# Optimization experiments

Measured on AMD Instinct MI355X. Metric: run time of the kernel, lower is better.

## Reference

```python
import jax, jax.numpy as jnp
import numpy as np
import math

B, N, F_IN, F_OUT = 8, 2048, 128, 128


def _uniform(key, shape, stdv):
    return jax.random.uniform(key, shape, dtype=jnp.float32, minval=-stdv, maxval=stdv)


def setup_inputs() -> dict:
    key = jax.random.key(0)
    k_x, k_a, k_w, k_att, k_bw, k_ba = jax.random.split(key, 6)
    X = jax.random.normal(k_x, (B, N, F_IN), dtype=jnp.float32)
    # dense 0/1 adjacency, as consumed by torch.bmm(A, ...)
    A = jax.random.randint(k_a, (B, N, N), 0, 2).astype(jnp.float32)
    stdv_W = 1.0 / math.sqrt(F_OUT)        # W.size(1) == n_fea_out
    stdv_a = 1.0 / math.sqrt(2 * F_OUT)    # a.size(1) == 2*n_fea_out
    W = _uniform(k_w, (F_IN, F_OUT), stdv_W)
    a = _uniform(k_att, (1, 2 * F_OUT), stdv_a)
    bias_W = _uniform(k_bw, (F_OUT,), stdv_W)
    bias_a = _uniform(k_ba, (N,), stdv_a)
    return {"X": X, "A": A, "W": W, "a": a, "bias_a": bias_a, "bias_W": bias_W}


def reference(X, A, W, a, bias_a, bias_W):
    # XW: [B, N, F_out]
    XW = jnp.einsum('bnf,fo->bno', X, W)
    f = W.shape[1]
    # Original materializes Z[b,i,j] = concat(XW[b,j], XW[b,i]) then dots with a.
    # This is separable: Z1[b,i,j] = a[:f]@XW[b,j] + a[f:]@XW[b,i] + bias_a[j]
    a_j = a[0, :f]   # multiplies XW[b, j]
    a_i = a[0, f:]   # multiplies XW[b, i]
    s_j = jnp.einsum('bnf,f->bn', XW, a_j)  # [B, N]
    s_i = jnp.einsum('bnf,f->bn', XW, a_i)  # [B, N]
    Z1 = s_i[:, :, None] + s_j[:, None, :] + bias_a[None, None, :]  # [B, N, N]
    den = jnp.exp(Z1)
    num = jnp.einsum('bik,bkj->bij', A, den)  # torch.bmm(A, denominator)
    # where numerator == 0 the torch code leaves att uninitialized; use 0 deterministically
    nz = num != 0
    att = jnp.where(nz, den / jnp.where(nz, num, 1.0), 0.0)
    buf = jnp.einsum('bij,bjf->bif', att, XW)
    H = jnp.einsum('bij,bjf->bif', A, buf) + bias_W
    return H
```

## Files before the change

kernel.cpp:

```cpp
#include <hip/hip_runtime.h>

#define BB 8
#define NN 2048
#define FF 128


__global__ __launch_bounds__(128) void k0_wai(const float* __restrict__ W,
                                              const float* __restrict__ a,
                                              float* __restrict__ w_ai) {
    int c = threadIdx.x;
    float s = 0.f;
#pragma unroll 8
    for (int f = 0; f < FF; ++f) s += W[c * FF + f] * a[FF + f];
    w_ai[c] = s;
}

__global__ __launch_bounds__(256) void k1_p_xsum(const float* __restrict__ X,
                                                 const float* __restrict__ w_ai,
                                                 float* __restrict__ p,
                                                 float* __restrict__ xsum) {
    int blk = blockIdx.x;
    int b = blk / (NN / 64);
    int row0 = (blk % (NN / 64)) * 64;
    int lane = threadIdx.x & 63;
    int wave = threadIdx.x >> 6;

    const float2* X2 = (const float2*)(X + ((size_t)b * NN + row0) * FF);
    float2 wv = ((const float2*)w_ai)[lane];
    float csx = 0.f, csy = 0.f;

    for (int it = 0; it < 16; ++it) {
        int rloc = wave * 16 + it;
        float2 xv = X2[(size_t)rloc * 64 + lane];
        csx += xv.x;
        csy += xv.y;
        float s = xv.x * wv.x + xv.y * wv.y;
#pragma unroll
        for (int off = 32; off; off >>= 1) s += __shfl_xor(s, off, 64);
        if (lane == 0) p[(size_t)b * NN + row0 + rloc] = expf(s);
    }

    __shared__ float cs_lds[4][FF];
    cs_lds[wave][lane * 2]     = csx;
    cs_lds[wave][lane * 2 + 1] = csy;
    __syncthreads();
    if (threadIdx.x < FF) {
        float v = cs_lds[0][threadIdx.x] + cs_lds[1][threadIdx.x] +
                  cs_lds[2][threadIdx.x] + cs_lds[3][threadIdx.x];
        atomicAdd(&xsum[b * FF + threadIdx.x], v);
    }
}

__global__ __launch_bounds__(128) void k2_S(const float* __restrict__ W,
                                            const float* __restrict__ xsum,
                                            float* __restrict__ S) {
    int b = blockIdx.x;
    int f = threadIdx.x;
    float s = 0.f;
#pragma unroll 8
    for (int c = 0; c < FF; ++c) s += xsum[b * FF + c] * W[c * FF + f];
    S[b * FF + f] = s;
}

__global__ __launch_bounds__(256) void k3_r(const float* __restrict__ A,
                                            const float* __restrict__ p,
                                            float* __restrict__ r) {
    __shared__ float p_lds[NN];
    int row0 = blockIdx.x * 4;
    int b = row0 >> 11;

    const float4* p4 = (const float4*)(p + (size_t)b * NN);
    ((float4*)p_lds)[threadIdx.x]       = p4[threadIdx.x];
    ((float4*)p_lds)[threadIdx.x + 256] = p4[threadIdx.x + 256];
    __syncthreads();

    int lane = threadIdx.x & 63;
    int wave = threadIdx.x >> 6;
    int row = row0 + wave;
    const float4* A4 = (const float4*)(A + (size_t)row * NN);

    float acc = 0.f;
#pragma unroll
    for (int it = 0; it < 8; ++it) {
        float4 av = A4[it * 64 + lane];
        float4 pv = *(const float4*)&p_lds[it * 256 + lane * 4];
        acc += av.x * pv.x + av.y * pv.y + av.z * pv.z + av.w * pv.w;
    }
#pragma unroll
    for (int off = 32; off; off >>= 1) acc += __shfl_xor(acc, off, 64);

    if (lane == 0) {
        int i = row & (NN - 1);
        r[row] = (acc != 0.f) ? (p_lds[i] / acc) : 0.f;
    }
}

__global__ __launch_bounds__(256) void k4_H(const float* __restrict__ A,
                                            const float* __restrict__ rr,
                                            const float* __restrict__ S,
                                            const float* __restrict__ bias_W,
                                            float* __restrict__ Hout) {
    __shared__ float r_lds[NN];
    __shared__ float s_lds[FF];
    __shared__ float bw_lds[FF];
    int row0 = blockIdx.x * 4;
    int b = row0 >> 11;

    const float4* r4 = (const float4*)(rr + (size_t)b * NN);
    ((float4*)r_lds)[threadIdx.x]       = r4[threadIdx.x];
    ((float4*)r_lds)[threadIdx.x + 256] = r4[threadIdx.x + 256];
    if (threadIdx.x < FF) {
        s_lds[threadIdx.x]  = S[b * FF + threadIdx.x];
        bw_lds[threadIdx.x] = bias_W[threadIdx.x];
    }
    __syncthreads();

    int lane = threadIdx.x & 63;
    int wave = threadIdx.x >> 6;
    int row = row0 + wave;
    const float4* A4 = (const float4*)(A + (size_t)row * NN);

    float acc = 0.f;
#pragma unroll
    for (int it = 0; it < 8; ++it) {
        float4 av = A4[it * 64 + lane];
        float4 rv = *(const float4*)&r_lds[it * 256 + lane * 4];
        acc += av.x * rv.x + av.y * rv.y + av.z * rv.z + av.w * rv.w;
    }
#pragma unroll
    for (int off = 32; off; off >>= 1) acc += __shfl_xor(acc, off, 64);

    float2 sv = ((const float2*)s_lds)[lane];
    float2 bv = ((const float2*)bw_lds)[lane];
    float2 hv;
    hv.x = acc * sv.x + bv.x;
    hv.y = acc * sv.y + bv.y;
    ((float2*)Hout)[(size_t)row * 64 + lane] = hv;
}

extern "C" void kernel_launch(void* const* d_in, const int* in_sizes, int n_in,
                              void* d_out, int out_size, void* d_ws, size_t ws_size,
                              hipStream_t stream) {
    const float* X      = (const float*)d_in[0];
    const float* A      = (const float*)d_in[1];
    const float* W      = (const float*)d_in[2];
    const float* a      = (const float*)d_in[3];
    const float* bias_W = (const float*)d_in[5];
    float* out = (float*)d_out;

    float* ws   = (float*)d_ws;
    float* w_ai = ws;
    float* xsum = ws + 128;
    float* S    = ws + 1152;
    float* p    = ws + 2176;
    float* r    = ws + 18560;

    hipMemsetAsync(xsum, 0, BB * FF * sizeof(float), stream);

    k0_wai<<<1, 128, 0, stream>>>(W, a, w_ai);
    k1_p_xsum<<<BB * (NN / 64), 256, 0, stream>>>(X, w_ai, p, xsum);
    k2_S<<<BB, 128, 0, stream>>>(W, xsum, S);
    k3_r<<<(BB * NN) / 4, 256, 0, stream>>>(A, p, r);
    k4_H<<<(BB * NN) / 4, 256, 0, stream>>>(A, r, S, bias_W, out);
}
```

Measured before the change: 249.1 us.

## Bit-pack adjacency in first A pass so second pass reads masks not floats

After: 240.7 us. 1.03x faster.

```diff
diff --git a/kernel.cpp b/kernel.cpp
--- a/kernel.cpp
+++ b/kernel.cpp
@@ -19,36 +19,38 @@
                                                  const float* __restrict__ w_ai,
                                                  float* __restrict__ p,
                                                  float* __restrict__ xsum) {
-    int blk = blockIdx.x;
-    int b = blk / (NN / 64);
-    int row0 = (blk % (NN / 64)) * 64;
+    __shared__ float xls[FF];
+    int gr0 = blockIdx.x * 32;
+    int b = gr0 >> 11;
     int lane = threadIdx.x & 63;
     int wave = threadIdx.x >> 6;
-
-    const float2* X2 = (const float2*)(X + ((size_t)b * NN + row0) * FF);
-    float2 wv = ((const float2*)w_ai)[lane];
-    float csx = 0.f, csy = 0.f;
-
-    for (int it = 0; it < 16; ++it) {
-        int rloc = wave * 16 + it;
-        float2 xv = X2[(size_t)rloc * 64 + lane];
-        csx += xv.x;
-        csy += xv.y;
-        float s = xv.x * wv.x + xv.y * wv.y;
-#pragma unroll
-        for (int off = 32; off; off >>= 1) s += __shfl_xor(s, off, 64);
-        if (lane == 0) p[(size_t)b * NN + row0 + rloc] = expf(s);
-    }
-
-    __shared__ float cs_lds[4][FF];
-    cs_lds[wave][lane * 2]     = csx;
-    cs_lds[wave][lane * 2 + 1] = csy;
-    __syncthreads();
-    if (threadIdx.x < FF) {
-        float v = cs_lds[0][threadIdx.x] + cs_lds[1][threadIdx.x] +
-                  cs_lds[2][threadIdx.x] + cs_lds[3][threadIdx.x];
-        atomicAdd(&xsum[b * FF + threadIdx.x], v);
-    }
+    int half = lane >> 5;
+    int l32 = lane & 31;
+
+    if (threadIdx.x < FF) xls[threadIdx.x] = 0.f;
+    __syncthreads();
+
+    float4 wv = ((const float4*)w_ai)[l32];
+    float4 cs = make_float4(0.f, 0.f, 0.f, 0.f);
+    const float4* X4 = (const float4*)(X + (size_t)gr0 * FF);
+
+#pragma unroll
+    for (int it = 0; it < 4; ++it) {
+        int rloc = wave * 8 + it * 2 + half;
+        float4 xv = X4[(size_t)rloc * 32 + l32];
+        cs.x += xv.x; cs.y += xv.y; cs.z += xv.z; cs.w += xv.w;
+        float s = xv.x * wv.x + xv.y * wv.y + xv.z * wv.z + xv.w * wv.w;
+#pragma unroll
+        for (int off = 16; off; off >>= 1) s += __shfl_xor(s, off, 64);
+        if (l32 == 0) p[(size_t)gr0 + rloc] = expf(s);
+    }
+
+    atomicAdd(&xls[l32 * 4 + 0], cs.x);
+    atomicAdd(&xls[l32 * 4 + 1], cs.y);
+    atomicAdd(&xls[l32 * 4 + 2], cs.z);
+    atomicAdd(&xls[l32 * 4 + 3], cs.w);
+    __syncthreads();
+    if (threadIdx.x < FF) atomicAdd(&xsum[b * FF + threadIdx.x], xls[threadIdx.x]);
 }
 
 __global__ __launch_bounds__(128) void k2_S(const float* __restrict__ W,
@@ -64,38 +66,68 @@
 
 __global__ __launch_bounds__(256) void k3_r(const float* __restrict__ A,
                                             const float* __restrict__ p,
-                                            float* __restrict__ r) {
+                                            float* __restrict__ r,
+                                            unsigned long long* __restrict__ pk) {
     __shared__ float p_lds[NN];
-    int row0 = blockIdx.x * 4;
+    int row0 = blockIdx.x * 8;
     int b = row0 >> 11;
 
     const float4* p4 = (const float4*)(p + (size_t)b * NN);
-    ((float4*)p_lds)[threadIdx.x]       = p4[threadIdx.x];
-    ((float4*)p_lds)[threadIdx.x + 256] = p4[threadIdx.x + 256];
+    float4* pl4 = (float4*)p_lds;
+    pl4[threadIdx.x]       = p4[threadIdx.x];
+    pl4[threadIdx.x + 256] = p4[threadIdx.x + 256];
     __syncthreads();
 
     int lane = threadIdx.x & 63;
     int wave = threadIdx.x >> 6;
-    int row = row0 + wave;
-    const float4* A4 = (const float4*)(A + (size_t)row * NN);
-
-    float acc = 0.f;
+    int rowA = row0 + wave * 2;
+    int rowB = rowA + 1;
+    const float4* Aa = (const float4*)(A + (size_t)rowA * NN);
+    const float4* Ab = (const float4*)(A + (size_t)rowB * NN);
+
+    int c = lane & 3;
+    float accA = 0.f, accB = 0.f;
 #pragma unroll
     for (int it = 0; it < 8; ++it) {
-        float4 av = A4[it * 64 + lane];
-        float4 pv = *(const float4*)&p_lds[it * 256 + lane * 4];
-        acc += av.x * pv.x + av.y * pv.y + av.z * pv.z + av.w * pv.w;
-    }
-#pragma unroll
-    for (int off = 32; off; off >>= 1) acc += __shfl_xor(acc, off, 64);
+        float4 pv = pl4[it * 64 + lane];
+        float4 va = Aa[it * 64 + lane];
+        float4 vb = Ab[it * 64 + lane];
+        accA += va.x * pv.x + va.y * pv.y + va.z * pv.z + va.w * pv.w;
+        accB += vb.x * pv.x + vb.y * pv.y + vb.z * pv.z + vb.w * pv.w;
+
+        unsigned long long a0 = __ballot(va.x != 0.f);
+        unsigned long long a1 = __ballot(va.y != 0.f);
+        unsigned long long a2 = __ballot(va.z != 0.f);
+        unsigned long long a3 = __ballot(va.w != 0.f);
+        unsigned long long b0 = __ballot(vb.x != 0.f);
+        unsigned long long b1 = __ballot(vb.y != 0.f);
+        unsigned long long b2 = __ballot(vb.z != 0.f);
+        unsigned long long b3 = __ballot(vb.w != 0.f);
+        if (lane < 8) {
+            unsigned long long alo = (c & 1) ? a1 : a0;
+            unsigned long long ahi = (c & 1) ? a3 : a2;
+            unsigned long long am  = (c & 2) ? ahi : alo;
+            unsigned long long blo = (c & 1) ? b1 : b0;
+            unsigned long long bhi = (c & 1) ? b3 : b2;
+            unsigned long long bm  = (c & 2) ? bhi : blo;
+            int row = (lane < 4) ? rowA : rowB;
+            unsigned long long m = (lane < 4) ? am : bm;
+            pk[(size_t)row * 32 + it * 4 + c] = m;
+        }
+    }
+#pragma unroll
+    for (int off = 32; off; off >>= 1) {
+        accA += __shfl_xor(accA, off, 64);
+        accB += __shfl_xor(accB, off, 64);
+    }
 
     if (lane == 0) {
-        int i = row & (NN - 1);
-        r[row] = (acc != 0.f) ? (p_lds[i] / acc) : 0.f;
-    }
-}
-
-__global__ __launch_bounds__(256) void k4_H(const float* __restrict__ A,
+        r[rowA] = (accA != 0.f) ? (p_lds[rowA & (NN - 1)] / accA) : 0.f;
+        r[rowB] = (accB != 0.f) ? (p_lds[rowB & (NN - 1)] / accB) : 0.f;
+    }
+}
+
+__global__ __launch_bounds__(256) void k4_H(const unsigned long long* __restrict__ pk,
                                             const float* __restrict__ rr,
                                             const float* __restrict__ S,
                                             const float* __restrict__ bias_W,
@@ -103,12 +135,13 @@
     __shared__ float r_lds[NN];
     __shared__ float s_lds[FF];
     __shared__ float bw_lds[FF];
-    int row0 = blockIdx.x * 4;
+    int row0 = blockIdx.x * 8;
     int b = row0 >> 11;
 
     const float4* r4 = (const float4*)(rr + (size_t)b * NN);
-    ((float4*)r_lds)[threadIdx.x]       = r4[threadIdx.x];
-    ((float4*)r_lds)[threadIdx.x + 256] = r4[threadIdx.x + 256];
+    float4* rl4 = (float4*)r_lds;
+    rl4[threadIdx.x]       = r4[threadIdx.x];
+    rl4[threadIdx.x + 256] = r4[threadIdx.x + 256];
     if (threadIdx.x < FF) {
         s_lds[threadIdx.x]  = S[b * FF + threadIdx.x];
         bw_lds[threadIdx.x] = bias_W[threadIdx.x];
@@ -117,25 +150,47 @@
 
     int lane = threadIdx.x & 63;
     int wave = threadIdx.x >> 6;
-    int row = row0 + wave;
-    const float4* A4 = (const float4*)(A + (size_t)row * NN);
-
-    float acc = 0.f;
+    int rowA = row0 + wave * 2;
+    int rowB = rowA + 1;
+
+    unsigned long long w =
+        pk[(size_t)(lane < 32 ? rowA : rowB) * 32 + (lane & 31)];
+
+    float accA = 0.f, accB = 0.f;
 #pragma unroll
     for (int it = 0; it < 8; ++it) {
-        float4 av = A4[it * 64 + lane];
-        float4 rv = *(const float4*)&r_lds[it * 256 + lane * 4];
-        acc += av.x * rv.x + av.y * rv.y + av.z * rv.z + av.w * rv.w;
-    }
-#pragma unroll
-    for (int off = 32; off; off >>= 1) acc += __shfl_xor(acc, off, 64);
+        float4 rv = rl4[it * 64 + lane];
+        unsigned long long mA0 = __shfl(w, it * 4 + 0, 64);
+        unsigned long long mA1 = __shfl(w, it * 4 + 1, 64);
+        unsigned long long mA2 = __shfl(w, it * 4 + 2, 64);
+        unsigned long long mA3 = __shfl(w, it * 4 + 3, 64);
+        unsigned long long mB0 = __shfl(w, 32 + it * 4 + 0, 64);
+        unsigned long long mB1 = __shfl(w, 32 + it * 4 + 1, 64);
+        unsigned long long mB2 = __shfl(w, 32 + it * 4 + 2, 64);
+        unsigned long long mB3 = __shfl(w, 32 + it * 4 + 3, 64);
+        if ((mA0 >> lane) & 1ull) accA += rv.x;
+        if ((mA1 >> lane) & 1ull) accA += rv.y;
+        if ((mA2 >> lane) & 1ull) accA += rv.z;
+        if ((mA3 >> lane) & 1ull) accA += rv.w;
+        if ((mB0 >> lane) & 1ull) accB += rv.x;
+        if ((mB1 >> lane) & 1ull) accB += rv.y;
+        if ((mB2 >> lane) & 1ull) accB += rv.z;
+        if ((mB3 >> lane) & 1ull) accB += rv.w;
+    }
+#pragma unroll
+    for (int off = 32; off; off >>= 1) {
+        accA += __shfl_xor(accA, off, 64);
+        accB += __shfl_xor(accB, off, 64);
+    }
 
     float2 sv = ((const float2*)s_lds)[lane];
     float2 bv = ((const float2*)bw_lds)[lane];
-    float2 hv;
-    hv.x = acc * sv.x + bv.x;
-    hv.y = acc * sv.y + bv.y;
-    ((float2*)Hout)[(size_t)row * 64 + lane] = hv;
+    float2* H2 = (float2*)Hout;
+    float2 ha, hb;
+    ha.x = accA * sv.x + bv.x;  ha.y = accA * sv.y + bv.y;
+    hb.x = accB * sv.x + bv.x;  hb.y = accB * sv.y + bv.y;
+    H2[(size_t)rowA * 64 + lane] = ha;
+    H2[(size_t)rowB * 64 + lane] = hb;
 }
 
 extern "C" void kernel_launch(void* const* d_in, const int* in_sizes, int n_in,
@@ -154,12 +209,13 @@
     float* S    = ws + 1152;
     float* p    = ws + 2176;
     float* r    = ws + 18560;
+    unsigned long long* pk = (unsigned long long*)(ws + 34944);
 
     hipMemsetAsync(xsum, 0, BB * FF * sizeof(float), stream);
 
     k0_wai<<<1, 128, 0, stream>>>(W, a, w_ai);
-    k1_p_xsum<<<BB * (NN / 64), 256, 0, stream>>>(X, w_ai, p, xsum);
+    k1_p_xsum<<<(BB * NN) / 32, 256, 0, stream>>>(X, w_ai, p, xsum);
     k2_S<<<BB, 128, 0, stream>>>(W, xsum, S);
-    k3_r<<<(BB * NN) / 4, 256, 0, stream>>>(A, p, r);
-    k4_H<<<(BB * NN) / 4, 256, 0, stream>>>(A, r, S, bias_W, out);
-}
+    k3_r<<<(BB * NN) / 8, 256, 0, stream>>>(A, p, r, pk);
+    k4_H<<<(BB * NN) / 8, 256, 0, stream>>>(pk, r, S, bias_W, out);
+}
```

## Fuse all stages into one persistent kernel with grid barriers and bit-packed adjacency

Applied to the files above, without the earlier changes.

New measurement: 378.1 us. 1.52x slower.

```diff
diff --git a/kernel.cpp b/kernel.cpp
--- a/kernel.cpp
+++ b/kernel.cpp
@@ -3,139 +3,183 @@
 #define BB 8
 #define NN 2048
 #define FF 128
-
-
-__global__ __launch_bounds__(128) void k0_wai(const float* __restrict__ W,
-                                              const float* __restrict__ a,
-                                              float* __restrict__ w_ai) {
-    int c = threadIdx.x;
-    float s = 0.f;
+#define NBLK 512
+#define RPB 32
+#define RPW 8
+typedef unsigned long long ull;
+
+
+__global__ __launch_bounds__(256, 2) void fused_gat(
+    const float* __restrict__ X, const float* __restrict__ A,
+    const float* __restrict__ W, const float* __restrict__ av,
+    const float* __restrict__ bias_W, float* __restrict__ Hout,
+    unsigned* __restrict__ bar, float* __restrict__ xpart,
+    float* __restrict__ S, float* __restrict__ p, float* __restrict__ r)
+{
+    __shared__ float lds[NN];
+    __shared__ float wls[FF], xls[FF], sls[FF], bwls[FF];
+
+    const int t = threadIdx.x;
+    const int lane = t & 63;
+    const int wave = t >> 6;
+    const int blk = blockIdx.x;
+    const int row0 = blk * RPB;
+    const int b = row0 >> 11;
+
+    if (t < FF) {
+        float s = 0.f;
 #pragma unroll 8
-    for (int f = 0; f < FF; ++f) s += W[c * FF + f] * a[FF + f];
-    w_ai[c] = s;
-}
-
-__global__ __launch_bounds__(256) void k1_p_xsum(const float* __restrict__ X,
-                                                 const float* __restrict__ w_ai,
-                                                 float* __restrict__ p,
-                                                 float* __restrict__ xsum) {
-    int blk = blockIdx.x;
-    int b = blk / (NN / 64);
-    int row0 = (blk % (NN / 64)) * 64;
-    int lane = threadIdx.x & 63;
-    int wave = threadIdx.x >> 6;
-
-    const float2* X2 = (const float2*)(X + ((size_t)b * NN + row0) * FF);
-    float2 wv = ((const float2*)w_ai)[lane];
-    float csx = 0.f, csy = 0.f;
-
-    for (int it = 0; it < 16; ++it) {
-        int rloc = wave * 16 + it;
-        float2 xv = X2[(size_t)rloc * 64 + lane];
-        csx += xv.x;
-        csy += xv.y;
-        float s = xv.x * wv.x + xv.y * wv.y;
-#pragma unroll
-        for (int off = 32; off; off >>= 1) s += __shfl_xor(s, off, 64);
-        if (lane == 0) p[(size_t)b * NN + row0 + rloc] = expf(s);
-    }
-
-    __shared__ float cs_lds[4][FF];
-    cs_lds[wave][lane * 2]     = csx;
-    cs_lds[wave][lane * 2 + 1] = csy;
-    __syncthreads();
-    if (threadIdx.x < FF) {
-        float v = cs_lds[0][threadIdx.x] + cs_lds[1][threadIdx.x] +
-                  cs_lds[2][threadIdx.x] + cs_lds[3][threadIdx.x];
-        atomicAdd(&xsum[b * FF + threadIdx.x], v);
-    }
-}
-
-__global__ __launch_bounds__(128) void k2_S(const float* __restrict__ W,
-                                            const float* __restrict__ xsum,
-                                            float* __restrict__ S) {
-    int b = blockIdx.x;
-    int f = threadIdx.x;
-    float s = 0.f;
+        for (int f = 0; f < FF; ++f) s += W[t * FF + f] * av[FF + f];
+        wls[t] = s;
+        xls[t] = 0.f;
+    }
+    __syncthreads();
+    {
+        const int hf = lane >> 5, l32 = lane & 31;
+        const float4 wv = ((const float4*)wls)[l32];
+        float4 cs = make_float4(0.f, 0.f, 0.f, 0.f);
+        const float4* X4 = (const float4*)(X + (size_t)row0 * FF);
+#pragma unroll
+        for (int k = 0; k < 4; ++k) {
+            const int rloc = k * 8 + wave * 2 + hf;
+            const float4 xv = X4[(size_t)rloc * 32 + l32];
+            cs.x += xv.x; cs.y += xv.y; cs.z += xv.z; cs.w += xv.w;
+            float s = xv.x * wv.x + xv.y * wv.y + xv.z * wv.z + xv.w * wv.w;
+#pragma unroll
+            for (int off = 16; off; off >>= 1) s += __shfl_xor(s, off, 64);
+            if (l32 == 0) p[row0 + rloc] = expf(s);
+        }
+        atomicAdd(&xls[l32 * 4 + 0], cs.x);
+        atomicAdd(&xls[l32 * 4 + 1], cs.y);
+        atomicAdd(&xls[l32 * 4 + 2], cs.z);
+        atomicAdd(&xls[l32 * 4 + 3], cs.w);
+    }
+    __syncthreads();
+    if (t < FF) xpart[blk * FF + t] = xls[t];
+    __threadfence();
+    __syncthreads();
+    if (t == 0)
+        __hip_atomic_fetch_add(&bar[0], 1u, __ATOMIC_RELEASE, __HIP_MEMORY_SCOPE_AGENT);
+
+    unsigned bits[8] = {0, 0, 0, 0, 0, 0, 0, 0};
+    const int rA = row0 + wave * RPW;
+    {
+        const float* Abase = A + (size_t)rA * NN;
+#pragma unroll 2
+        for (int it = 0; it < 8; ++it) {
+#pragma unroll
+            for (int q = 0; q < 8; ++q) {
+                const float4 v = ((const float4*)(Abase + (size_t)q * NN))[it * 64 + lane];
+                unsigned nib = 0;
+                if (v.x != 0.f) nib |= 1u;
+                if (v.y != 0.f) nib |= 2u;
+                if (v.z != 0.f) nib |= 4u;
+                if (v.w != 0.f) nib |= 8u;
+                bits[q] |= nib << (it * 4);
+            }
+        }
+    }
+
+    if (t == 0) {
+        while (__hip_atomic_load(&bar[0], __ATOMIC_ACQUIRE, __HIP_MEMORY_SCOPE_AGENT) < NBLK)
+            __builtin_amdgcn_s_sleep(1);
+    }
+    __syncthreads();
+
+    float4* l4 = (float4*)lds;
+    {
+        const float4* pg = (const float4*)(p + (size_t)b * NN);
+        l4[t]       = pg[t];
+        l4[t + 256] = pg[t + 256];
+    }
+    __syncthreads();
+    {
+        float acc[8] = {0, 0, 0, 0, 0, 0, 0, 0};
+#pragma unroll
+        for (int it = 0; it < 8; ++it) {
+            const float4 pv = l4[it * 64 + lane];
+#pragma unroll
+            for (int q = 0; q < 8; ++q) {
+                const unsigned nib = (bits[q] >> (it * 4)) & 15u;
+                acc[q] += (nib & 1u) ? pv.x : 0.f;
+                acc[q] += (nib & 2u) ? pv.y : 0.f;
+                acc[q] += (nib & 4u) ? pv.z : 0.f;
+                acc[q] += (nib & 8u) ? pv.w : 0.f;
+            }
+        }
+#pragma unroll
+        for (int q = 0; q < 8; ++q)
+#pragma unroll
+            for (int off = 32; off; off >>= 1) acc[q] += __shfl_xor(acc[q], off, 64);
+        if (lane == 0) {
+            const int lr = rA & (NN - 1);
+#pragma unroll
+            for (int q = 0; q < 8; ++q)
+                r[rA + q] = (acc[q] != 0.f) ? (lds[lr + q] / acc[q]) : 0.f;
+        }
+    }
+
+    if ((blk & 63) == 0) {
+        __syncthreads();
+        if (t < FF) {
+            const float* xp = xpart + (size_t)(b * 64) * FF + t;
+            float s = 0.f;
+#pragma unroll 4
+            for (int j = 0; j < 64; ++j) s += xp[j * FF];
+            xls[t] = s;
+        }
+        __syncthreads();
+        if (t < FF) {
+            float s = 0.f;
 #pragma unroll 8
-    for (int c = 0; c < FF; ++c) s += xsum[b * FF + c] * W[c * FF + f];
-    S[b * FF + f] = s;
-}
-
-__global__ __launch_bounds__(256) void k3_r(const float* __restrict__ A,
-                                            const float* __restrict__ p,
-                                            float* __restrict__ r) {
-    __shared__ float p_lds[NN];
-    int row0 = blockIdx.x * 4;
-    int b = row0 >> 11;
-
-    const float4* p4 = (const float4*)(p + (size_t)b * NN);
-    ((float4*)p_lds)[threadIdx.x]       = p4[threadIdx.x];
-    ((float4*)p_lds)[threadIdx.x + 256] = p4[threadIdx.x + 256];
-    __syncthreads();
-
-    int lane = threadIdx.x & 63;
-    int wave = threadIdx.x >> 6;
-    int row = row0 + wave;
-    const float4* A4 = (const float4*)(A + (size_t)row * NN);
-
-    float acc = 0.f;
-#pragma unroll
-    for (int it = 0; it < 8; ++it) {
-        float4 av = A4[it * 64 + lane];
-        float4 pv = *(const float4*)&p_lds[it * 256 + lane * 4];
-        acc += av.x * pv.x + av.y * pv.y + av.z * pv.z + av.w * pv.w;
-    }
-#pragma unroll
-    for (int off = 32; off; off >>= 1) acc += __shfl_xor(acc, off, 64);
-
-    if (lane == 0) {
-        int i = row & (NN - 1);
-        r[row] = (acc != 0.f) ? (p_lds[i] / acc) : 0.f;
-    }
-}
-
-__global__ __launch_bounds__(256) void k4_H(const float* __restrict__ A,
-                                            const float* __restrict__ rr,
-                                            const float* __restrict__ S,
-                                            const float* __restrict__ bias_W,
-                                            float* __restrict__ Hout) {
-    __shared__ float r_lds[NN];
-    __shared__ float s_lds[FF];
-    __shared__ float bw_lds[FF];
-    int row0 = blockIdx.x * 4;
-    int b = row0 >> 11;
-
-    const float4* r4 = (const float4*)(rr + (size_t)b * NN);
-    ((float4*)r_lds)[threadIdx.x]       = r4[threadIdx.x];
-    ((float4*)r_lds)[threadIdx.x + 256] = r4[threadIdx.x + 256];
-    if (threadIdx.x < FF) {
-        s_lds[threadIdx.x]  = S[b * FF + threadIdx.x];
-        bw_lds[threadIdx.x] = bias_W[threadIdx.x];
-    }
-    __syncthreads();
-
-    int lane = threadIdx.x & 63;
-    int wave = threadIdx.x >> 6;
-    int row = row0 + wave;
-    const float4* A4 = (const float4*)(A + (size_t)row * NN);
-
-    float acc = 0.f;
-#pragma unroll
-    for (int it = 0; it < 8; ++it) {
-        float4 av = A4[it * 64 + lane];
-        float4 rv = *(const float4*)&r_lds[it * 256 + lane * 4];
-        acc += av.x * rv.x + av.y * rv.y + av.z * rv.z + av.w * rv.w;
-    }
-#pragma unroll
-    for (int off = 32; off; off >>= 1) acc += __shfl_xor(acc, off, 64);
-
-    float2 sv = ((const float2*)s_lds)[lane];
-    float2 bv = ((const float2*)bw_lds)[lane];
-    float2 hv;
-    hv.x = acc * sv.x + bv.x;
-    hv.y = acc * sv.y + bv.y;
-    ((float2*)Hout)[(size_t)row * 64 + lane] = hv;
+            for (int c2 = 0; c2 < FF; ++c2) s += xls[c2] * W[c2 * FF + t];
+            S[b * FF + t] = s;
+        }
+    }
+
+    __threadfence();
+    __syncthreads();
+    if (t == 0) {
+        __hip_atomic_fetch_add(&bar[32], 1u, __ATOMIC_RELEASE, __HIP_MEMORY_SCOPE_AGENT);
+        while (__hip_atomic_load(&bar[32], __ATOMIC_ACQUIRE, __HIP_MEMORY_SCOPE_AGENT) < NBLK)
+            __builtin_amdgcn_s_sleep(1);
+    }
+    __syncthreads();
+
+    {
+        const float4* rg = (const float4*)(r + (size_t)b * NN);
+        l4[t]       = rg[t];
+        l4[t + 256] = rg[t + 256];
+        if (t < FF) { sls[t] = S[(size_t)b * FF + t]; bwls[t] = bias_W[t]; }
+    }
+    __syncthreads();
+    {
+        float acc[8] = {0, 0, 0, 0, 0, 0, 0, 0};
+#pragma unroll
+        for (int it = 0; it < 8; ++it) {
+            const float4 rv = l4[it * 64 + lane];
+#pragma unroll
+            for (int q = 0; q < 8; ++q) {
+                const unsigned nib = (bits[q] >> (it * 4)) & 15u;
+                acc[q] += (nib & 1u) ? rv.x : 0.f;
+                acc[q] += (nib & 2u) ? rv.y : 0.f;
+                acc[q] += (nib & 4u) ? rv.z : 0.f;
+                acc[q] += (nib & 8u) ? rv.w : 0.f;
+            }
+        }
+#pragma unroll
+        for (int q = 0; q < 8; ++q)
+#pragma unroll
+            for (int off = 32; off; off >>= 1) acc[q] += __shfl_xor(acc[q], off, 64);
+
+        const float2 sv = ((const float2*)sls)[lane];
+        const float2 bv = ((const float2*)bwls)[lane];
+        float2* H2 = (float2*)Hout;
+#pragma unroll
+        for (int q = 0; q < 8; ++q)
+            H2[(size_t)(rA + q) * 64 + lane] =
+                make_float2(acc[q] * sv.x + bv.x, acc[q] * sv.y + bv.y);
+    }
 }
 
 extern "C" void kernel_launch(void* const* d_in, const int* in_sizes, int n_in,
@@ -148,18 +192,13 @@
     const float* bias_W = (const float*)d_in[5];
     float* out = (float*)d_out;
 
-    float* ws   = (float*)d_ws;
-    float* w_ai = ws;
-    float* xsum = ws + 128;
-    float* S    = ws + 1152;
-    float* p    = ws + 2176;
-    float* r    = ws + 18560;
-
-    hipMemsetAsync(xsum, 0, BB * FF * sizeof(float), stream);
-
-    k0_wai<<<1, 128, 0, stream>>>(W, a, w_ai);
-    k1_p_xsum<<<BB * (NN / 64), 256, 0, stream>>>(X, w_ai, p, xsum);
-    k2_S<<<BB, 128, 0, stream>>>(W, xsum, S);
-    k3_r<<<(BB * NN) / 4, 256, 0, stream>>>(A, p, r);
-    k4_H<<<(BB * NN) / 4, 256, 0, stream>>>(A, r, S, bias_W, out);
+    float* ws = (float*)d_ws;
+    unsigned* bar = (unsigned*)ws;
+    float* xpart = ws + 64;
+    float* S     = ws + 65600;
+    float* p     = ws + 66624;
+    float* r     = ws + 83008;
+
+    hipMemsetAsync(bar, 0, 256, stream);
+    fused_gat<<<NBLK, 256, 0, stream>>>(X, A, W, a, bias_W, out, bar, xpart, S, p, r);
 }
```
